# Performance work log

Measured on AMD Instinct MI355X. Metric: run time of the kernel, lower is better.

## Reference

```python
import jax, jax.numpy as jnp
import numpy as np

N_ATOMS = 500_000
N_MOLS = 25_000
HID = 300
CONSTRAINT = 0.0  # per-molecule target total (e.g. neutral net charge)
W_SCALE = 0.05    # keep random-init activations tame


def setup_inputs() -> dict:
    key = jax.random.key(0)
    ks = jax.random.split(key, 6)
    hidden = jax.random.normal(ks[0], (N_ATOMS, HID), dtype=jnp.float32)
    seg_ids = jnp.sort(jax.random.randint(ks[1], (N_ATOMS,), 0, N_MOLS, dtype=jnp.int32))
    # output readout FFN: Linear(300->300) -> ReLU -> Linear(300->1)
    W1 = jax.random.normal(ks[2], (HID, HID), dtype=jnp.float32) * W_SCALE
    b1 = jnp.zeros((HID,), dtype=jnp.float32)
    W2 = jax.random.normal(ks[3], (HID, 1), dtype=jnp.float32) * W_SCALE
    b2 = jnp.zeros((1,), dtype=jnp.float32)
    # weights readout FFN (same architecture); bias=1 keeps segment weight sums positive
    V1 = jax.random.normal(ks[4], (HID, HID), dtype=jnp.float32) * W_SCALE
    vb1 = jnp.zeros((HID,), dtype=jnp.float32)
    V2 = jax.random.normal(ks[5], (HID, 1), dtype=jnp.float32) * W_SCALE
    vb2 = jnp.ones((1,), dtype=jnp.float32)
    return {"hidden": hidden, "seg_ids": seg_ids, "W1": W1, "b1": b1, "W2": W2,
            "b2": b2, "V1": V1, "vb1": vb1, "V2": V2, "vb2": vb2}


def _ffn(x, Wa, ba, Wb, bb):
    # dropout is identity in eval mode
    h = jax.nn.relu(x @ Wa + ba)
    return h @ Wb + bb  # [N, 1]


def reference(hidden, seg_ids, W1, b1, W2, b2, V1, vb1, V2, vb2):
    output = _ffn(hidden, W1, b1, W2, b2)    # [N, 1] raw per-atom predictions
    weights = _ffn(hidden, V1, vb1, V2, vb2) # [N, 1] per-atom correction weights
    # per-molecule segment sums (replaces the Python loop over a_scope)
    sum_o = jax.ops.segment_sum(output[:, 0], seg_ids, num_segments=N_MOLS)   # [M]
    sum_w = jax.ops.segment_sum(weights[:, 0], seg_ids, num_segments=N_MOLS)  # [M]
    sum_w = jnp.where(sum_w == 0, 1.0, sum_w)  # empty segments are skipped in the original
    corr = (CONSTRAINT - sum_o) / sum_w        # [M]
    out = output + weights * corr[seg_ids][:, None]  # [N, 1]
    return out
```

## Files before the change

kernel.cpp:

```cpp
#include <hip/hip_runtime.h>
#include <stdint.h>

#define N_ATOMS 500000
#define N_MOLS  25000
#define HID     300
#define BA      64
#define WS_ELE  102400
#define NCH     19

#define A_OFF   0
#define AROW    40
#define B_OFF   2560
#define BUFSZ   23040

typedef __attribute__((ext_vector_type(8)))  short          short8v;
typedef __attribute__((ext_vector_type(16))) float          f32x16;

static __device__ __forceinline__ unsigned short f2bf(float f) {
  unsigned int u = __float_as_uint(f);
  u += 0x7fffu + ((u >> 16) & 1u);
  return (unsigned short)(u >> 16);
}

static __device__ __forceinline__ void stage16(const char* gsrc, char* ldst, int ln) {
  __builtin_amdgcn_global_load_lds(
      (const __attribute__((address_space(1))) void*)(gsrc + ln * 16),
      (__attribute__((address_space(3))) void*)ldst, 16, 0, 0);
}

__global__ void prep_kernel(
    const float* __restrict__ W1, const float* __restrict__ V1,
    const float* __restrict__ b1, const float* __restrict__ vb1,
    const float* __restrict__ W2, const float* __restrict__ V2,
    unsigned short* __restrict__ W1s, unsigned short* __restrict__ V1s,
    float* __restrict__ b1p, float* __restrict__ vb1p,
    float* __restrict__ W2p, float* __restrict__ V2p,
    float* __restrict__ sums)
{
  const int t = blockIdx.x * 256 + threadIdx.x;
  if (t < 2 * WS_ELE) {
    const float* src = (t < WS_ELE) ? W1 : V1;
    unsigned short* dst = (t < WS_ELE) ? W1s : V1s;
    const int i    = (t < WS_ELE) ? t : t - WS_ELE;
    const int j    = i & 7;
    const int lane = (i >> 3) & 63;
    const int nt   = (i >> 9) % 10;
    const int kc16 = i / 5120;
    const int k = kc16 * 16 + (lane >> 5) * 8 + j;
    const int n = nt * 32 + (lane & 31);
    const float v = (k < HID && n < HID) ? src[k * HID + n] : 0.f;
    dst[i] = f2bf(v);
  } else if (t < 2 * WS_ELE + 1280) {
    const int i = t - 2 * WS_ELE;
    const int which = i / 320;
    const int e = i - which * 320;
    const float* s = (which == 0) ? b1 : (which == 1) ? vb1 : (which == 2) ? W2 : V2;
    float*       d = (which == 0) ? b1p : (which == 1) ? vb1p : (which == 2) ? W2p : V2p;
    d[e] = (e < HID) ? s[e] : 0.f;
  } else if (t < 2 * WS_ELE + 1280 + 2 * N_MOLS) {
    sums[t - (2 * WS_ELE + 1280)] = 0.f;
  }
}

__global__ __launch_bounds__(512, 4) void fused_ffn(
    const float* __restrict__ hidden,
    const unsigned short* __restrict__ W1s, const unsigned short* __restrict__ V1s,
    const float* __restrict__ b1p, const float* __restrict__ vb1p,
    const float* __restrict__ W2p, const float* __restrict__ V2p,
    const float* __restrict__ b2, const float* __restrict__ vb2,
    float* __restrict__ outA, float* __restrict__ outW)
{
  __shared__ char lds[2 * BUFSZ];
  __shared__ float sOutA[BA];
  __shared__ float sOutW[BA];

  const int tid = (int)threadIdx.x;
  const int ln  = tid & 63;
  const int wv  = tid >> 6;
  const int mtx = wv & 1;
  const int wn  = (wv >> 1) & 1;
  const int wm  = wv >> 2;
  const int l31 = ln & 31;
  const int lh  = ln >> 5;
  const long base = (long)blockIdx.x * BA;

  const int sa  = tid >> 3;
  const int skk = (tid & 7) * 2;
  const long satom = base + sa;
  const bool aok = satom < N_ATOMS;
  const float* srow = hidden + (aok ? satom : 0) * (long)HID;

  const float bias2A = b2[0];
  const float bias2W = vb2[0];

  f32x16 acc[5] = {};

  {
    const int k = skk;
    float2 av = make_float2(0.f, 0.f);
    if (aok) av = *reinterpret_cast<const float2*>(srow + k);
    #pragma unroll
    for (int r = 0; r < 3; ++r) {
      const int c = r * 8 + wv;
      if (c < 20) {
        const char* src = (c < 10) ? ((const char*)W1s + c * 1024)
                                   : ((const char*)V1s + (c - 10) * 1024);
        stage16(src, lds + B_OFF + c * 1024, ln);
      }
    }
    ushort2 bv; bv.x = f2bf(av.x); bv.y = f2bf(av.y);
    *reinterpret_cast<ushort2*>(lds + A_OFF + sa * AROW + skk * 2) = bv;
  }
  __syncthreads();

  for (int c = 0; c < NCH; ++c) {
    const int cur = c & 1;
    const char* cbuf = lds + cur * BUFSZ;
    char*       nbuf = lds + (cur ^ 1) * BUFSZ;

    float2 av = make_float2(0.f, 0.f);
    if (c < NCH - 1) {
      const int k = (c + 1) * 16 + skk;
      if (aok && k < HID) av = *reinterpret_cast<const float2*>(srow + k);
      const char* wsrc = (const char*)W1s + (c + 1) * 10240;
      const char* vsrc = (const char*)V1s + (c + 1) * 10240;
      #pragma unroll
      for (int r = 0; r < 3; ++r) {
        const int cc = r * 8 + wv;
        if (cc < 20) {
          const char* src = (cc < 10) ? (wsrc + cc * 1024) : (vsrc + (cc - 10) * 1024);
          stage16(src, nbuf + B_OFF + cc * 1024, ln);
        }
      }
    }

    const short8v af = *reinterpret_cast<const short8v*>(
        cbuf + A_OFF + (wm * 32 + l31) * AROW + lh * 16);
    const char* bbase = cbuf + B_OFF + mtx * 10240;
    #pragma unroll
    for (int nt = 0; nt < 5; ++nt) {
      const short8v bf = *reinterpret_cast<const short8v*>(
          bbase + (wn * 5 + nt) * 1024 + ln * 16);
      acc[nt] = __builtin_amdgcn_mfma_f32_32x32x16_bf16(af, bf, acc[nt], 0, 0, 0);
    }

    if (c < NCH - 1) {
      ushort2 bv; bv.x = f2bf(av.x); bv.y = f2bf(av.y);
      *reinterpret_cast<ushort2*>(nbuf + A_OFF + sa * AROW + skk * 2) = bv;
    }
    __syncthreads();
  }

  float bv[5], w2[5];
  const float* bbv = mtx ? vb1p : b1p;
  const float* ww2 = mtx ? V2p  : W2p;
  #pragma unroll
  for (int nt = 0; nt < 5; ++nt) {
    const int cix = wn * 160 + nt * 32 + l31;
    bv[nt] = bbv[cix];
    w2[nt] = ww2[cix];
  }
  if (tid < BA) { sOutA[tid] = 0.f; sOutW[tid] = 0.f; }
  __syncthreads();

  float* sOut = mtx ? sOutW : sOutA;
  #pragma unroll
  for (int r = 0; r < 16; ++r) {
    float s = 0.f;
    #pragma unroll
    for (int nt = 0; nt < 5; ++nt) {
      float x = fmaxf(acc[nt][r] + bv[nt], 0.f);
      s = fmaf(x, w2[nt], s);
    }
    s += __shfl_xor(s, 1);
    s += __shfl_xor(s, 2);
    s += __shfl_xor(s, 4);
    s += __shfl_xor(s, 8);
    s += __shfl_xor(s, 16);
    if (l31 == 0) {
      const int row = (r & 3) + 8 * (r >> 2) + 4 * lh;
      atomicAdd(&sOut[wm * 32 + row], s);
    }
  }
  __syncthreads();
  if (tid < BA) {
    const long atom = base + tid;
    if (atom < N_ATOMS) {
      outA[atom] = sOutA[tid] + bias2A;
      outW[atom] = sOutW[tid] + bias2W;
    }
  }
}

__global__ void segsum_kernel(
    const float* __restrict__ outA, const float* __restrict__ outW,
    const int* __restrict__ seg,
    float* __restrict__ sum_o, float* __restrict__ sum_w)
{
  const long i0 = ((long)blockIdx.x * 256 + threadIdx.x) * 8;
  if (i0 >= N_ATOMS) return;
  const int4   s0 = *reinterpret_cast<const int4*>(seg + i0);
  const int4   s1 = *reinterpret_cast<const int4*>(seg + i0 + 4);
  const float4 o0 = *reinterpret_cast<const float4*>(outA + i0);
  const float4 o1 = *reinterpret_cast<const float4*>(outA + i0 + 4);
  const float4 w0 = *reinterpret_cast<const float4*>(outW + i0);
  const float4 w1 = *reinterpret_cast<const float4*>(outW + i0 + 4);
  const int   ss[8] = {s0.x, s0.y, s0.z, s0.w, s1.x, s1.y, s1.z, s1.w};
  const float oo[8] = {o0.x, o0.y, o0.z, o0.w, o1.x, o1.y, o1.z, o1.w};
  const float ww[8] = {w0.x, w0.y, w0.z, w0.w, w1.x, w1.y, w1.z, w1.w};
  int cur = ss[0];
  float ao = 0.f, aw = 0.f;
  #pragma unroll
  for (int j = 0; j < 8; ++j) {
    if (ss[j] != cur) {
      atomicAdd(&sum_o[cur], ao);
      atomicAdd(&sum_w[cur], aw);
      cur = ss[j]; ao = 0.f; aw = 0.f;
    }
    ao += oo[j]; aw += ww[j];
  }
  atomicAdd(&sum_o[cur], ao);
  atomicAdd(&sum_w[cur], aw);
}

__global__ void final_kernel(
    const float* __restrict__ outA, const float* __restrict__ outW,
    const int* __restrict__ seg,
    const float* __restrict__ sum_o, const float* __restrict__ sum_w,
    float* __restrict__ out)
{
  const long i0 = ((long)blockIdx.x * 256 + threadIdx.x) * 4;
  if (i0 >= N_ATOMS) return;
  const int4   s4 = *reinterpret_cast<const int4*>(seg + i0);
  const float4 o4 = *reinterpret_cast<const float4*>(outA + i0);
  const float4 w4 = *reinterpret_cast<const float4*>(outW + i0);
  const int   ss[4] = {s4.x, s4.y, s4.z, s4.w};
  const float oo[4] = {o4.x, o4.y, o4.z, o4.w};
  const float ww[4] = {w4.x, w4.y, w4.z, w4.w};
  float r[4];
  #pragma unroll
  for (int j = 0; j < 4; ++j) {
    const int s = ss[j];
    float sw = sum_w[s];
    sw = (sw == 0.f) ? 1.f : sw;
    const float corr = (0.f - sum_o[s]) / sw;
    r[j] = oo[j] + ww[j] * corr;
  }
  *reinterpret_cast<float4*>(out + i0) = make_float4(r[0], r[1], r[2], r[3]);
}

extern "C" void kernel_launch(void* const* d_in, const int* in_sizes, int n_in,
                              void* d_out, int out_size, void* d_ws, size_t ws_size,
                              hipStream_t stream)
{
  const float* hidden = (const float*)d_in[0];
  const int*   seg    = (const int*)d_in[1];
  const float* W1     = (const float*)d_in[2];
  const float* b1     = (const float*)d_in[3];
  const float* W2     = (const float*)d_in[4];
  const float* b2     = (const float*)d_in[5];
  const float* V1     = (const float*)d_in[6];
  const float* vb1    = (const float*)d_in[7];
  const float* V2     = (const float*)d_in[8];
  const float* vb2    = (const float*)d_in[9];

  char* ws = (char*)d_ws;
  float*          outA  = (float*)(ws + 0);
  float*          outW  = (float*)(ws + 2000000);
  float*          sum_o = (float*)(ws + 4000000);
  float*          sum_w = (float*)(ws + 4100000);
  unsigned short* W1s   = (unsigned short*)(ws + 4200000);
  unsigned short* V1s   = (unsigned short*)(ws + 4404800);
  float*          b1p   = (float*)(ws + 4609600);
  float*          vb1p  = (float*)(ws + 4610880);
  float*          W2p   = (float*)(ws + 4612160);
  float*          V2p   = (float*)(ws + 4613440);

  prep_kernel<<<1001, 256, 0, stream>>>(W1, V1, b1, vb1, W2, V2,
                                        W1s, V1s, b1p, vb1p, W2p, V2p, sum_o);

  const int nblk = (N_ATOMS + BA - 1) / BA;
  fused_ffn<<<nblk, 512, 0, stream>>>(hidden, W1s, V1s, b1p, vb1p, W2p, V2p,
                                      b2, vb2, outA, outW);

  segsum_kernel<<<(N_ATOMS / 8 + 255) / 256, 256, 0, stream>>>(outA, outW, seg,
                                                               sum_o, sum_w);

  final_kernel<<<(N_ATOMS / 4 + 255) / 256, 256, 0, stream>>>(outA, outW, seg,
                                                              sum_o, sum_w,
                                                              (float*)d_out);
}
```

Measured before the change: 476.2 us.

## Preload whole A tile into LDS and double atom tile per block

The fused FFN kernel now processes 128 atoms per block instead of 64. It loads the entire bf16-converted hidden tile into LDS up front with coalesced float4 loads, then streams the weight tiles two k16 chunks at a time with double buffering, so there are 10 iterations instead of 19. Each wave computes two 32-row M tiles against the same B fragments, which doubles weight reuse and halves barrier count per FLOP. The cost is a larger LDS footprint (about 160KB), and launch bounds drop to 2 blocks per CU, which lowers occupancy and may expose the upfront load latency.

```diff
diff --git a/kernel.cpp b/kernel.cpp
--- a/kernel.cpp
+++ b/kernel.cpp
@@ -4,14 +4,13 @@
 #define N_ATOMS 500000
 #define N_MOLS  25000
 #define HID     300
-#define BA      64
+#define BA      128
 #define WS_ELE  102400
-#define NCH     19
-
-#define A_OFF   0
-#define AROW    40
-#define B_OFF   2560
-#define BUFSZ   23040
+
+#define NK16    19
+#define A_BYTES (NK16 * 4096)
+#define B_OFF   A_BYTES
+#define BUF_B   40960
 
 typedef __attribute__((ext_vector_type(8)))  short          short8v;
 typedef __attribute__((ext_vector_type(16))) float          f32x16;
@@ -62,7 +61,7 @@
   }
 }
 
-__global__ __launch_bounds__(512, 4) void fused_ffn(
+__global__ __launch_bounds__(512, 2) void fused_ffn(
     const float* __restrict__ hidden,
     const unsigned short* __restrict__ W1s, const unsigned short* __restrict__ V1s,
     const float* __restrict__ b1p, const float* __restrict__ vb1p,
@@ -70,7 +69,7 @@
     const float* __restrict__ b2, const float* __restrict__ vb2,
     float* __restrict__ outA, float* __restrict__ outW)
 {
-  __shared__ char lds[2 * BUFSZ];
+  __shared__ char lds[A_BYTES + 2 * BUF_B];
   __shared__ float sOutA[BA];
   __shared__ float sOutW[BA];
 
@@ -78,76 +77,96 @@
   const int ln  = tid & 63;
   const int wv  = tid >> 6;
   const int mtx = wv & 1;
-  const int wn  = (wv >> 1) & 1;
-  const int wm  = wv >> 2;
+  const int ch  = (wv >> 1) & 1;
+  const int rgh = wv >> 2;
   const int l31 = ln & 31;
   const int lh  = ln >> 5;
   const long base = (long)blockIdx.x * BA;
 
-  const int sa  = tid >> 3;
-  const int skk = (tid & 7) * 2;
-  const long satom = base + sa;
-  const bool aok = satom < N_ATOMS;
-  const float* srow = hidden + (aok ? satom : 0) * (long)HID;
-
-  const float bias2A = b2[0];
-  const float bias2W = vb2[0];
-
-  f32x16 acc[5] = {};
-
   {
-    const int k = skk;
-    float2 av = make_float2(0.f, 0.f);
-    if (aok) av = *reinterpret_cast<const float2*>(srow + k);
+    char* dst = lds + B_OFF;
     #pragma unroll
-    for (int r = 0; r < 3; ++r) {
-      const int c = r * 8 + wv;
-      if (c < 20) {
-        const char* src = (c < 10) ? ((const char*)W1s + c * 1024)
-                                   : ((const char*)V1s + (c - 10) * 1024);
-        stage16(src, lds + B_OFF + c * 1024, ln);
+    for (int r = 0; r < 5; ++r) {
+      const int cc = wv * 5 + r;
+      const char* src = (cc < 20) ? ((const char*)W1s + cc * 1024)
+                                  : ((const char*)V1s + (cc - 20) * 1024);
+      stage16(src, dst + cc * 1024, ln);
+    }
+  }
+
+  float4 ld[19];
+  const bool tail = (tid >= 384);
+  #pragma unroll
+  for (int j = 0; j < 19; ++j) {
+    const int i = tid + j * 512;
+    const int row = i / 75;
+    const int c4  = i - row * 75;
+    float4 v = make_float4(0.f, 0.f, 0.f, 0.f);
+    const long atom = base + row;
+    if ((j < 18 || !tail) && atom < N_ATOMS)
+      v = *reinterpret_cast<const float4*>(hidden + atom * (long)HID + c4 * 4);
+    ld[j] = v;
+  }
+  #pragma unroll
+  for (int j = 0; j < 19; ++j) {
+    if (j == 18 && tail) break;
+    const int i   = tid + j * 512;
+    const int row = i / 75;
+    const int c4  = i - row * 75;
+    const int k   = c4 * 4;
+    const int k16 = k >> 4;
+    const int sub = k & 15;
+    ushort4 b;
+    b.x = f2bf(ld[j].x); b.y = f2bf(ld[j].y);
+    b.z = f2bf(ld[j].z); b.w = f2bf(ld[j].w);
+    char* p = lds + k16 * 4096 + (row >> 5) * 1024
+            + (((row & 31) + ((sub >> 3) << 5)) * 16) + (sub & 7) * 2;
+    *reinterpret_cast<ushort4*>(p) = b;
+  }
+  if (tail) {
+    const int row = tid - 384;
+    char* p = lds + 18 * 4096 + (row >> 5) * 1024 + (((row & 31) + 32) * 16) + 8;
+    *reinterpret_cast<ushort4*>(p) = make_ushort4(0, 0, 0, 0);
+  }
+  __syncthreads();
+
+  f32x16 acc[2][5] = {};
+
+  for (int c = 0; c < 10; ++c) {
+    const char* buf = lds + B_OFF + (c & 1) * BUF_B;
+
+    if (c < 9) {
+      char* nbuf = lds + B_OFF + ((c + 1) & 1) * BUF_B;
+      const char* wsrc = (const char*)W1s + (c + 1) * 20480;
+      const char* vsrc = (const char*)V1s + (c + 1) * 20480;
+      #pragma unroll
+      for (int r = 0; r < 5; ++r) {
+        const int cc = wv * 5 + r;
+        const char* src = (cc < 20) ? (wsrc + cc * 1024) : (vsrc + (cc - 20) * 1024);
+        stage16(src, nbuf + cc * 1024, ln);
       }
     }
-    ushort2 bv; bv.x = f2bf(av.x); bv.y = f2bf(av.y);
-    *reinterpret_cast<ushort2*>(lds + A_OFF + sa * AROW + skk * 2) = bv;
-  }
-  __syncthreads();
-
-  for (int c = 0; c < NCH; ++c) {
-    const int cur = c & 1;
-    const char* cbuf = lds + cur * BUFSZ;
-    char*       nbuf = lds + (cur ^ 1) * BUFSZ;
-
-    float2 av = make_float2(0.f, 0.f);
-    if (c < NCH - 1) {
-      const int k = (c + 1) * 16 + skk;
-      if (aok && k < HID) av = *reinterpret_cast<const float2*>(srow + k);
-      const char* wsrc = (const char*)W1s + (c + 1) * 10240;
-      const char* vsrc = (const char*)V1s + (c + 1) * 10240;
-      #pragma unroll
-      for (int r = 0; r < 3; ++r) {
-        const int cc = r * 8 + wv;
-        if (cc < 20) {
-          const char* src = (cc < 10) ? (wsrc + cc * 1024) : (vsrc + (cc - 10) * 1024);
-          stage16(src, nbuf + B_OFF + cc * 1024, ln);
-        }
-      }
-    }
-
-    const short8v af = *reinterpret_cast<const short8v*>(
-        cbuf + A_OFF + (wm * 32 + l31) * AROW + lh * 16);
-    const char* bbase = cbuf + B_OFF + mtx * 10240;
-    #pragma unroll
-    for (int nt = 0; nt < 5; ++nt) {
-      const short8v bf = *reinterpret_cast<const short8v*>(
-          bbase + (wn * 5 + nt) * 1024 + ln * 16);
-      acc[nt] = __builtin_amdgcn_mfma_f32_32x32x16_bf16(af, bf, acc[nt], 0, 0, 0);
-    }
-
-    if (c < NCH - 1) {
-      ushort2 bv; bv.x = f2bf(av.x); bv.y = f2bf(av.y);
-      *reinterpret_cast<ushort2*>(nbuf + A_OFF + sa * AROW + skk * 2) = bv;
-    }
+
+#define DO_HALF(hh)                                                            \
+    {                                                                          \
+      const int kc16 = 2 * c + (hh);                                           \
+      const short8v a0 = *reinterpret_cast<const short8v*>(                    \
+          lds + kc16 * 4096 + (rgh * 2 + 0) * 1024 + ln * 16);                 \
+      const short8v a1 = *reinterpret_cast<const short8v*>(                    \
+          lds + kc16 * 4096 + (rgh * 2 + 1) * 1024 + ln * 16);                 \
+      const char* bb = buf + mtx * 20480 + (hh) * 10240 + ch * 5120;           \
+      _Pragma("unroll")                                                        \
+      for (int nt = 0; nt < 5; ++nt) {                                         \
+        const short8v bf = *reinterpret_cast<const short8v*>(                  \
+            bb + nt * 1024 + ln * 16);                                         \
+        acc[0][nt] = __builtin_amdgcn_mfma_f32_32x32x16_bf16(a0, bf, acc[0][nt], 0, 0, 0); \
+        acc[1][nt] = __builtin_amdgcn_mfma_f32_32x32x16_bf16(a1, bf, acc[1][nt], 0, 0, 0); \
+      }                                                                        \
+    }
+    DO_HALF(0);
+    if (c < 9) DO_HALF(1);
+#undef DO_HALF
+
     __syncthreads();
   }
 
@@ -156,7 +175,7 @@
   const float* ww2 = mtx ? V2p  : W2p;
   #pragma unroll
   for (int nt = 0; nt < 5; ++nt) {
-    const int cix = wn * 160 + nt * 32 + l31;
+    const int cix = ch * 160 + nt * 32 + l31;
     bv[nt] = bbv[cix];
     w2[nt] = ww2[cix];
   }
@@ -165,29 +184,32 @@
 
   float* sOut = mtx ? sOutW : sOutA;
   #pragma unroll
-  for (int r = 0; r < 16; ++r) {
-    float s = 0.f;
+  for (int rg = 0; rg < 2; ++rg) {
     #pragma unroll
-    for (int nt = 0; nt < 5; ++nt) {
-      float x = fmaxf(acc[nt][r] + bv[nt], 0.f);
-      s = fmaf(x, w2[nt], s);
-    }
-    s += __shfl_xor(s, 1);
-    s += __shfl_xor(s, 2);
-    s += __shfl_xor(s, 4);
-    s += __shfl_xor(s, 8);
-    s += __shfl_xor(s, 16);
-    if (l31 == 0) {
-      const int row = (r & 3) + 8 * (r >> 2) + 4 * lh;
-      atomicAdd(&sOut[wm * 32 + row], s);
+    for (int r = 0; r < 16; ++r) {
+      float s = 0.f;
+      #pragma unroll
+      for (int nt = 0; nt < 5; ++nt) {
+        float x = fmaxf(acc[rg][nt][r] + bv[nt], 0.f);
+        s = fmaf(x, w2[nt], s);
+      }
+      s += __shfl_xor(s, 1);
+      s += __shfl_xor(s, 2);
+      s += __shfl_xor(s, 4);
+      s += __shfl_xor(s, 8);
+      s += __shfl_xor(s, 16);
+      if (l31 == 0) {
+        const int row = rgh * 64 + rg * 32 + (r & 3) + 8 * (r >> 2) + 4 * lh;
+        atomicAdd(&sOut[row], s);
+      }
     }
   }
   __syncthreads();
   if (tid < BA) {
     const long atom = base + tid;
     if (atom < N_ATOMS) {
-      outA[atom] = sOutA[tid] + bias2A;
-      outW[atom] = sOutW[tid] + bias2W;
+      outA[atom] = sOutA[tid] + b2[0];
+      outW[atom] = sOutW[tid] + vb2[0];
     }
   }
 }
```

New measurement: 648.7 us. 36.2% more time.

## Load A fragments directly from global into registers, skipping LDS staging

Applied to the files above, without the earlier changes.

Each lane now reads its own hidden-row fragment (8 floats as two float4s) straight from global memory and converts it to bf16 in registers for the MFMA A operand. This removes the LDS write, LDS read and the A region of each buffer. Weight-slab staging is also redistributed unevenly across waves, with 3 or 2 slabs per wave. In exchange, four waves (two matrices times two column halves) each load the same hidden rows redundantly, so global/L2 traffic on the activation rises.

```diff
diff --git a/kernel.cpp b/kernel.cpp
--- a/kernel.cpp
+++ b/kernel.cpp
@@ -7,11 +7,7 @@
 #define BA      64
 #define WS_ELE  102400
 #define NCH     19
-
-#define A_OFF   0
-#define AROW    40
-#define B_OFF   2560
-#define BUFSZ   23040
+#define SLAB    20480
 
 typedef __attribute__((ext_vector_type(8)))  short          short8v;
 typedef __attribute__((ext_vector_type(16))) float          f32x16;
@@ -20,6 +16,26 @@
   unsigned int u = __float_as_uint(f);
   u += 0x7fffu + ((u >> 16) & 1u);
   return (unsigned short)(u >> 16);
+}
+
+static __device__ __forceinline__ short8v pack8(float4 a, float4 b) {
+  short8v r;
+  r[0] = (short)f2bf(a.x); r[1] = (short)f2bf(a.y);
+  r[2] = (short)f2bf(a.z); r[3] = (short)f2bf(a.w);
+  r[4] = (short)f2bf(b.x); r[5] = (short)f2bf(b.y);
+  r[6] = (short)f2bf(b.z); r[7] = (short)f2bf(b.w);
+  return r;
+}
+
+static __device__ __forceinline__ void loadA(const float* hp, int k0,
+                                             float4& f0, float4& f1) {
+  if (k0 <= 288) {
+    f0 = *reinterpret_cast<const float4*>(hp + k0);
+    f1 = *reinterpret_cast<const float4*>(hp + k0 + 4);
+  } else {
+    f0 = *reinterpret_cast<const float4*>(hp + 296);
+    f1 = make_float4(0.f, 0.f, 0.f, 0.f);
+  }
 }
 
 static __device__ __forceinline__ void stage16(const char* gsrc, char* ldst, int ln) {
@@ -70,7 +86,7 @@
     const float* __restrict__ b2, const float* __restrict__ vb2,
     float* __restrict__ outA, float* __restrict__ outW)
 {
-  __shared__ char lds[2 * BUFSZ];
+  __shared__ char lds[2 * SLAB];
   __shared__ float sOutA[BA];
   __shared__ float sOutW[BA];
 
@@ -78,76 +94,62 @@
   const int ln  = tid & 63;
   const int wv  = tid >> 6;
   const int mtx = wv & 1;
-  const int wn  = (wv >> 1) & 1;
-  const int wm  = wv >> 2;
+  const int ch  = (wv >> 1) & 1;
+  const int rg  = wv >> 2;
   const int l31 = ln & 31;
   const int lh  = ln >> 5;
   const long base = (long)blockIdx.x * BA;
 
-  const int sa  = tid >> 3;
-  const int skk = (tid & 7) * 2;
-  const long satom = base + sa;
-  const bool aok = satom < N_ATOMS;
-  const float* srow = hidden + (aok ? satom : 0) * (long)HID;
-
-  const float bias2A = b2[0];
-  const float bias2W = vb2[0];
+  long rowl = base + rg * 32 + l31;
+  if (rowl > N_ATOMS - 1) rowl = N_ATOMS - 1;
+  const float* hp = hidden + rowl * (long)HID;
+
+  const int p0 = (wv < 4) ? wv * 3 : 12 + (wv - 4) * 2;
+  const int np = (wv < 4) ? 3 : 2;
 
   f32x16 acc[5] = {};
 
-  {
-    const int k = skk;
-    float2 av = make_float2(0.f, 0.f);
-    if (aok) av = *reinterpret_cast<const float2*>(srow + k);
-    #pragma unroll
-    for (int r = 0; r < 3; ++r) {
-      const int c = r * 8 + wv;
-      if (c < 20) {
-        const char* src = (c < 10) ? ((const char*)W1s + c * 1024)
-                                   : ((const char*)V1s + (c - 10) * 1024);
-        stage16(src, lds + B_OFF + c * 1024, ln);
-      }
-    }
-    ushort2 bv; bv.x = f2bf(av.x); bv.y = f2bf(av.y);
-    *reinterpret_cast<ushort2*>(lds + A_OFF + sa * AROW + skk * 2) = bv;
+  float4 c0, c1;
+  loadA(hp, lh * 8, c0, c1);
+  #pragma unroll
+  for (int r = 0; r < 3; ++r) {
+    if (r < np) {
+      const int c = p0 + r;
+      const char* src = (c < 10) ? ((const char*)W1s + c * 1024)
+                                 : ((const char*)V1s + (c - 10) * 1024);
+      stage16(src, lds + c * 1024, ln);
+    }
   }
   __syncthreads();
 
   for (int c = 0; c < NCH; ++c) {
-    const int cur = c & 1;
-    const char* cbuf = lds + cur * BUFSZ;
-    char*       nbuf = lds + (cur ^ 1) * BUFSZ;
-
-    float2 av = make_float2(0.f, 0.f);
+    const char* buf = lds + (c & 1) * SLAB;
+
+    float4 n0, n1;
     if (c < NCH - 1) {
-      const int k = (c + 1) * 16 + skk;
-      if (aok && k < HID) av = *reinterpret_cast<const float2*>(srow + k);
+      loadA(hp, (c + 1) * 16 + lh * 8, n0, n1);
+      char* nbuf = lds + ((c + 1) & 1) * SLAB;
       const char* wsrc = (const char*)W1s + (c + 1) * 10240;
       const char* vsrc = (const char*)V1s + (c + 1) * 10240;
       #pragma unroll
       for (int r = 0; r < 3; ++r) {
-        const int cc = r * 8 + wv;
-        if (cc < 20) {
+        if (r < np) {
+          const int cc = p0 + r;
           const char* src = (cc < 10) ? (wsrc + cc * 1024) : (vsrc + (cc - 10) * 1024);
-          stage16(src, nbuf + B_OFF + cc * 1024, ln);
+          stage16(src, nbuf + cc * 1024, ln);
         }
       }
     }
 
-    const short8v af = *reinterpret_cast<const short8v*>(
-        cbuf + A_OFF + (wm * 32 + l31) * AROW + lh * 16);
-    const char* bbase = cbuf + B_OFF + mtx * 10240;
+    const short8v af = pack8(c0, c1);
+    const char* bb = buf + mtx * 10240 + ch * 5120;
     #pragma unroll
     for (int nt = 0; nt < 5; ++nt) {
-      const short8v bf = *reinterpret_cast<const short8v*>(
-          bbase + (wn * 5 + nt) * 1024 + ln * 16);
+      const short8v bf = *reinterpret_cast<const short8v*>(bb + nt * 1024 + ln * 16);
       acc[nt] = __builtin_amdgcn_mfma_f32_32x32x16_bf16(af, bf, acc[nt], 0, 0, 0);
     }
 
-    if (c < NCH - 1) {
-      ushort2 bv; bv.x = f2bf(av.x); bv.y = f2bf(av.y);
-      *reinterpret_cast<ushort2*>(nbuf + A_OFF + sa * AROW + skk * 2) = bv;
-    }
+    if (c < NCH - 1) { c0 = n0; c1 = n1; }
     __syncthreads();
   }
 
@@ -156,7 +158,7 @@
   const float* ww2 = mtx ? V2p  : W2p;
   #pragma unroll
   for (int nt = 0; nt < 5; ++nt) {
-    const int cix = wn * 160 + nt * 32 + l31;
+    const int cix = ch * 160 + nt * 32 + l31;
     bv[nt] = bbv[cix];
     w2[nt] = ww2[cix];
   }
@@ -178,16 +180,16 @@
     s += __shfl_xor(s, 8);
     s += __shfl_xor(s, 16);
     if (l31 == 0) {
-      const int row = (r & 3) + 8 * (r >> 2) + 4 * lh;
-      atomicAdd(&sOut[wm * 32 + row], s);
+      const int row = rg * 32 + (r & 3) + 8 * (r >> 2) + 4 * lh;
+      atomicAdd(&sOut[row], s);
     }
   }
   __syncthreads();
   if (tid < BA) {
     const long atom = base + tid;
     if (atom < N_ATOMS) {
-      outA[atom] = sOutA[tid] + bias2A;
-      outW[atom] = sOutW[tid] + bias2W;
+      outA[atom] = sOutA[tid] + b2[0];
+      outW[atom] = sOutW[tid] + vb2[0];
     }
   }
 }
```

New measurement: 474.4 us. No clear change (-0.4%).
